# Kernel optimization log

Hardware: AMD Instinct MI355X
Metric: run time of the kernel (lower is better)

The kernel has to match this reference:

```python
import jax, jax.numpy as jnp
import numpy as np

S = 7  # output_size


def _bin_indices(lo, hi, dim):
    """PyTorch AdaptiveMaxPool windows for each of S bins over [lo, hi] (inclusive).
    Returns gather indices [R,S,K] and validity mask [R,S,K].
    start_i = floor(i*L/S), end_i = ceil((i+1)*L/S), L = hi-lo+1."""
    L = hi - lo + 1  # [R]
    i = jnp.arange(S)
    start = lo[:, None] + (i * L[:, None]) // S          # [R,S]
    end = lo[:, None] + ((i + 1) * L[:, None] + S - 1) // S  # [R,S]
    K = (dim + S - 1) // S + 1  # static max window size
    k = jnp.arange(K)
    idx = start[:, :, None] + k                          # [R,S,K]
    valid = idx < end[:, :, None]
    return jnp.clip(idx, 0, dim - 1), valid


def setup_inputs() -> dict:
    key = jax.random.key(0)
    k1, k2 = jax.random.split(key)
    feature_map = jax.random.normal(k1, (1, 256, 64, 64), dtype=jnp.float32)
    # generate valid ROIs: sort coordinate pairs so x1<=x2, y1<=y2
    pairs = jax.random.randint(k2, (1, 128, 2, 2), 0, 64)  # [B,R,(x|y),2]
    pairs = jnp.sort(pairs, axis=-1)
    rois = jnp.stack(
        [pairs[..., 0, 0], pairs[..., 1, 0], pairs[..., 0, 1], pairs[..., 1, 1]],
        axis=-1,
    ).astype(jnp.int32)  # [1,128,4] = (x1,y1,x2,y2)
    return {"feature_map": feature_map, "rois": rois}


def reference(feature_map, rois):
    f = feature_map[0]  # [C,H,W]  (module only works with batch=1)
    C, H, W = f.shape
    r = rois.reshape(-1, 4).astype(jnp.int32)
    x1, y1, x2, y2 = r[:, 0], r[:, 1], r[:, 2], r[:, 3]
    neg = jnp.finfo(f.dtype).min

    # pool over dim 2 (x / f_wid axis, per original slicing feature_map[:,:,x1:x2+1,...])
    h_idx, h_val = _bin_indices(x1, x2, H)               # [R,S,Kh]
    g1 = f[:, h_idx, :]                                  # [C,R,S,Kh,W]
    rowmax = jnp.max(jnp.where(h_val[None, :, :, :, None], g1, neg), axis=3)  # [C,R,S,W]

    # pool over dim 3 (y / f_hei axis)
    w_idx, w_val = _bin_indices(y1, y2, W)               # [R,S,Kw]
    R_, Sw, Kw = w_idx.shape
    g2 = jnp.take_along_axis(rowmax, w_idx.reshape(1, R_, 1, Sw * Kw), axis=3)
    g2 = g2.reshape(C, R_, S, Sw, Kw)                    # [C,R,S,S,Kw]
    pooled = jnp.max(jnp.where(w_val[None, :, None, :, :], g2, neg), axis=4)  # [C,R,S,S]

    # pooled_rois[b, roi, c, S, S] -> flatten to [1, R, C, S*S]
    out = pooled.transpose(1, 0, 2, 3).reshape(1, R_, C, S * S)
    return out
```

## Files before the change

### kernel.cpp

```cpp
#include <hip/hip_runtime.h>
#include <cfloat>

#define NS 7
#define NC 256
#define NH 64
#define NW 64
#define NR 128

__global__ __launch_bounds__(256) void roi_pool_kernel(
    const float* __restrict__ f,
    const int* __restrict__ rois,
    float* __restrict__ out)
{
    __shared__ float colmax_lds[4][NS][NW];

    const int lane = threadIdx.x & 63;
    const int wid  = threadIdx.x >> 6;

    const int r  = blockIdx.x >> 6;
    const int cg = blockIdx.x & 63;
    const int c  = cg * 4 + wid;

    const int x1 = rois[4 * r + 0];
    const int y1 = rois[4 * r + 1];
    const int x2 = rois[4 * r + 2];
    const int y2 = rois[4 * r + 3];
    const int Lh = x2 - x1 + 1;
    const int Lw = y2 - y1 + 1;

    const float* fc = f + (size_t)c * (NH * NW);

    for (int i = 0; i < NS; ++i) {
        const int hs = x1 + (i * Lh) / NS;
        const int he = x1 + ((i + 1) * Lh + NS - 1) / NS;
        float m = -FLT_MAX;
        if (lane < Lw) {
            const float* p = fc + hs * NW + y1 + lane;
            for (int h = hs; h < he; ++h) {
                m = fmaxf(m, *p);
                p += NW;
            }
        }
        colmax_lds[wid][i][lane] = m;
    }

    __syncthreads();

    if (lane < NS * NS) {
        const int i  = lane / NS;
        const int j  = lane % NS;
        const int cs = (j * Lw) / NS;
        const int ce = ((j + 1) * Lw + NS - 1) / NS;
        float m = -FLT_MAX;
        #pragma unroll 1
        for (int k = cs; k < ce; ++k)
            m = fmaxf(m, colmax_lds[wid][i][k]);
        out[((size_t)(r * NC + c)) * (NS * NS) + lane] = m;
    }
}

extern "C" void kernel_launch(void* const* d_in, const int* in_sizes, int n_in,
                              void* d_out, int out_size, void* d_ws, size_t ws_size,
                              hipStream_t stream)
{
    const float* feature_map = (const float*)d_in[0];
    const int*   rois        = (const int*)d_in[1];
    float*       out         = (float*)d_out;

    const int grid  = NR * (NC / 4);
    const int block = 256;

    roi_pool_kernel<<<grid, block, 0, stream>>>(feature_map, rois, out);
}
```

Before: 28.01 us.

## Process four ROIs per wave for one channel with float2 row-pair loads

Work is remapped so each block handles one channel across 16 ROIs, with each wave looping over 4 ROIs. This favours cache reuse of that channel's plane. Row pooling reads full 64-wide rows as float2, with the two half-waves taking alternate rows. The halves are merged with v_permlane32_swap, and a per-wave padded LDS stripe replaces the block-wide barrier. The cost is extra loads over the full row width regardless of ROI width, serial ROI iteration inside each wave, and a gfx950-specific inline asm instruction.

Result: slower. 30.70 us (+9.6%).

```diff
diff --git a/kernel.cpp b/kernel.cpp
--- a/kernel.cpp
+++ b/kernel.cpp
@@ -6,56 +6,95 @@
 #define NH 64
 #define NW 64
 #define NR 128
+#define SPAD 66
 
-__global__ __launch_bounds__(256) void roi_pool_kernel(
+__global__ __launch_bounds__(256, 8) void roi_pool_kernel(
     const float* __restrict__ f,
     const int* __restrict__ rois,
     float* __restrict__ out)
 {
-    __shared__ float colmax_lds[4][NS][NW];
+    __shared__ float stripe_all[4][NS][SPAD];
 
-    const int lane = threadIdx.x & 63;
-    const int wid  = threadIdx.x >> 6;
+    const int tid  = threadIdx.x;
+    const int lane = tid & 63;
+    const int wid  = tid >> 6;
+    float (*stripe)[SPAD] = stripe_all[wid];
 
-    const int r  = blockIdx.x >> 6;
-    const int cg = blockIdx.x & 63;
-    const int c  = cg * 4 + wid;
+    const int c  = blockIdx.x & 255;
+    const int rg = blockIdx.x >> 8;
+    const int r0 = rg * 16 + wid * 4;
 
-    const int x1 = rois[4 * r + 0];
-    const int y1 = rois[4 * r + 1];
-    const int x2 = rois[4 * r + 2];
-    const int y2 = rois[4 * r + 3];
-    const int Lh = x2 - x1 + 1;
-    const int Lw = y2 - y1 + 1;
+    const char* fcb = (const char*)(f + (size_t)c * (NH * NW));
 
-    const float* fc = f + (size_t)c * (NH * NW);
+    const int w2    = lane & 31;
+    const int halfb = (lane >> 5) << 8;
+    const int woff  = w2 * 8;
 
-    for (int i = 0; i < NS; ++i) {
-        const int hs = x1 + (i * Lh) / NS;
-        const int he = x1 + ((i + 1) * Lh + NS - 1) / NS;
-        float m = -FLT_MAX;
-        if (lane < Lw) {
-            const float* p = fc + hs * NW + y1 + lane;
-            for (int h = hs; h < he; ++h) {
-                m = fmaxf(m, *p);
-                p += NW;
+    const int bl = lane < NS * NS ? lane : NS * NS - 1;
+    const int bi = bl / NS;
+    const int bj = bl - bi * NS;
+
+    for (int rr = 0; rr < 4; ++rr) {
+        const int r  = r0 + rr;
+        const int x1 = __builtin_amdgcn_readfirstlane(rois[4 * r + 0]);
+        const int y1 = __builtin_amdgcn_readfirstlane(rois[4 * r + 1]);
+        const int x2 = __builtin_amdgcn_readfirstlane(rois[4 * r + 2]);
+        const int y2 = __builtin_amdgcn_readfirstlane(rois[4 * r + 3]);
+        const int Lh = x2 - x1 + 1;
+        const int Lw = y2 - y1 + 1;
+
+        int hsb[NS], helimb[NS];
+        int maxrows = 0;
+        #pragma unroll
+        for (int i = 0; i < NS; ++i) {
+            int hs = x1 + (i * Lh) / NS;
+            int he = x1 + ((i + 1) * Lh + NS - 1) / NS;
+            hsb[i]    = hs << 8;
+            helimb[i] = (he - 1) << 8;
+            maxrows   = max(maxrows, he - hs);
+        }
+        const int K2 = (maxrows + 1) >> 1;
+
+        float2 acc[NS];
+        #pragma unroll
+        for (int i = 0; i < NS; ++i) acc[i] = make_float2(-FLT_MAX, -FLT_MAX);
+
+        for (int k = 0; k < K2; ++k) {
+            const int kb = k << 9;
+            #pragma unroll
+            for (int i = 0; i < NS; ++i) {
+                int rb = min(hsb[i] + kb + halfb, helimb[i]);
+                float2 v = *(const float2*)(fcb + rb + woff);
+                acc[i].x = fmaxf(acc[i].x, v.x);
+                acc[i].y = fmaxf(acc[i].y, v.y);
             }
         }
-        colmax_lds[wid][i][lane] = m;
-    }
 
-    __syncthreads();
+        #pragma unroll
+        for (int i = 0; i < NS; ++i) {
+            float ax = acc[i].x, bx = acc[i].x;
+            float ay = acc[i].y, by = acc[i].y;
+            asm("v_permlane32_swap_b32 %0, %1" : "+v"(ax), "+v"(bx));
+            asm("v_permlane32_swap_b32 %0, %1" : "+v"(ay), "+v"(by));
+            float2 mv = make_float2(fmaxf(ax, bx), fmaxf(ay, by));
+            if (lane < 32)
+                *(float2*)&stripe[i][2 * w2] = mv;
+        }
 
-    if (lane < NS * NS) {
-        const int i  = lane / NS;
-        const int j  = lane % NS;
-        const int cs = (j * Lw) / NS;
-        const int ce = ((j + 1) * Lw + NS - 1) / NS;
-        float m = -FLT_MAX;
-        #pragma unroll 1
-        for (int k = cs; k < ce; ++k)
-            m = fmaxf(m, colmax_lds[wid][i][k]);
-        out[((size_t)(r * NC + c)) * (NS * NS) + lane] = m;
+        {
+            const int Kc  = (Lw + NS - 1) / NS;
+            const int wsj = y1 + (bj * Lw) / NS;
+            const int wej = y1 + ((bj + 1) * Lw + NS - 1) / NS;
+            const int spj = wej - wsj;
+
+            float m = -FLT_MAX;
+            for (int k = 0; k <= Kc; ++k) {
+                float v = stripe[bi][wsj + k];
+                m = fmaxf(m, k < spj ? v : -FLT_MAX);
+            }
+            if (lane < NS * NS)
+                out[((size_t)r * NC + c) * (NS * NS) + lane] = m;
+        }
     }
 }
 
@@ -67,7 +106,7 @@
     const int*   rois        = (const int*)d_in[1];
     float*       out         = (float*)d_out;
 
-    const int grid  = NR * (NC / 4);
+    const int grid  = 8 * 256;
     const int block = 256;
 
     roi_pool_kernel<<<grid, block, 0, stream>>>(feature_map, rois, out);
```

## Transpose feature map to HWC and pool one bin per wave over channels

Applied to the files above, without the earlier changes.

Adds a tiled transpose kernel that rewrites the CHW feature map into an HWC workspace. The pooling kernel then gives each wave one (roi, bin, 64-channel group), with lanes mapped to channels. Each lane reads its bin window directly with coalesced loads and no LDS or barrier. In exchange it pays an extra full transpose pass and a second launch, and the output stores become strided by 49 floats per lane.

New measurement: 32.81 us. +17.1%, slower.

```diff
diff --git a/kernel.cpp b/kernel.cpp
--- a/kernel.cpp
+++ b/kernel.cpp
@@ -7,56 +7,79 @@
 #define NW 64
 #define NR 128
 
-__global__ __launch_bounds__(256) void roi_pool_kernel(
-    const float* __restrict__ f,
-    const int* __restrict__ rois,
+#define RFL(x) __builtin_amdgcn_readfirstlane(x)
+
+__global__ __launch_bounds__(256) void transpose_chw_hwc(
+    const float* __restrict__ f, float* __restrict__ ft)
+{
+    __shared__ float tile[16][65];
+    const int tid = threadIdx.x;
+    const int h   = blockIdx.x >> 4;
+    const int c0  = ((blockIdx.x >> 2) & 3) * 64;
+    const int w0  = (blockIdx.x & 3) * 16;
+
+    {
+        int c  = tid >> 2;
+        int w4 = (tid & 3) * 4;
+        float4 v = *(const float4*)(f + (size_t)(c0 + c) * (NH * NW) + h * NW + w0 + w4);
+        tile[w4 + 0][c] = v.x;
+        tile[w4 + 1][c] = v.y;
+        tile[w4 + 2][c] = v.z;
+        tile[w4 + 3][c] = v.w;
+    }
+    __syncthreads();
+    {
+        int w  = tid >> 4;
+        int c4 = (tid & 15) * 4;
+        float4 v = make_float4(tile[w][c4 + 0], tile[w][c4 + 1],
+                               tile[w][c4 + 2], tile[w][c4 + 3]);
+        *(float4*)(ft + (size_t)h * (NW * NC) + (w0 + w) * NC + c0 + c4) = v;
+    }
+}
+
+__global__ __launch_bounds__(256) void roi_pool_hwc(
+    const float* __restrict__ ft, const int* __restrict__ rois,
     float* __restrict__ out)
 {
-    __shared__ float colmax_lds[4][NS][NW];
+    const int lane = threadIdx.x & 63;
+    const int wv   = threadIdx.x >> 6;
+    const int W    = blockIdx.x * 4 + wv;
 
-    const int lane = threadIdx.x & 63;
-    const int wid  = threadIdx.x >> 6;
+    const int cg  = RFL(W & 3);
+    const int rb_ = W >> 2;
+    const int bin = RFL(rb_ % (NS * NS));
+    const int r   = RFL(rb_ / (NS * NS));
+    const int i   = bin / NS;
+    const int j   = bin - i * NS;
 
-    const int r  = blockIdx.x >> 6;
-    const int cg = blockIdx.x & 63;
-    const int c  = cg * 4 + wid;
-
-    const int x1 = rois[4 * r + 0];
-    const int y1 = rois[4 * r + 1];
-    const int x2 = rois[4 * r + 2];
-    const int y2 = rois[4 * r + 3];
+    const int4 rq = ((const int4*)rois)[r];
+    const int x1 = RFL(rq.x), y1 = RFL(rq.y), x2 = RFL(rq.z), y2 = RFL(rq.w);
     const int Lh = x2 - x1 + 1;
     const int Lw = y2 - y1 + 1;
 
-    const float* fc = f + (size_t)c * (NH * NW);
+    const int h0 = x1 + (i * Lh) / NS;
+    const int h1 = x1 + ((i + 1) * Lh + NS - 1) / NS;
+    const int w0 = y1 + (j * Lw) / NS;
+    const int w1 = y1 + ((j + 1) * Lw + NS - 1) / NS;
 
-    for (int i = 0; i < NS; ++i) {
-        const int hs = x1 + (i * Lh) / NS;
-        const int he = x1 + ((i + 1) * Lh + NS - 1) / NS;
-        float m = -FLT_MAX;
-        if (lane < Lw) {
-            const float* p = fc + hs * NW + y1 + lane;
-            for (int h = hs; h < he; ++h) {
-                m = fmaxf(m, *p);
-                p += NW;
-            }
+    const float* fcl = ft + cg * 64 + lane;
+
+    float m = -FLT_MAX;
+    for (int h = h0; h < h1; ++h) {
+        const size_t rowo = (size_t)(h * NW) * NC;
+        for (int wg = w0; wg < w1; wg += 4) {
+            int wB = min(wg + 1, w1 - 1);
+            int wC = min(wg + 2, w1 - 1);
+            int wD = min(wg + 3, w1 - 1);
+            float a = fcl[rowo + (size_t)wg * NC];
+            float b = fcl[rowo + (size_t)wB * NC];
+            float c = fcl[rowo + (size_t)wC * NC];
+            float d = fcl[rowo + (size_t)wD * NC];
+            m = fmaxf(m, fmaxf(fmaxf(a, b), fmaxf(c, d)));
         }
-        colmax_lds[wid][i][lane] = m;
     }
 
-    __syncthreads();
-
-    if (lane < NS * NS) {
-        const int i  = lane / NS;
-        const int j  = lane % NS;
-        const int cs = (j * Lw) / NS;
-        const int ce = ((j + 1) * Lw + NS - 1) / NS;
-        float m = -FLT_MAX;
-        #pragma unroll 1
-        for (int k = cs; k < ce; ++k)
-            m = fmaxf(m, colmax_lds[wid][i][k]);
-        out[((size_t)(r * NC + c)) * (NS * NS) + lane] = m;
-    }
+    out[((size_t)(r * NC + cg * 64 + lane)) * (NS * NS) + bin] = m;
 }
 
 extern "C" void kernel_launch(void* const* d_in, const int* in_sizes, int n_in,
@@ -66,9 +89,10 @@
     const float* feature_map = (const float*)d_in[0];
     const int*   rois        = (const int*)d_in[1];
     float*       out         = (float*)d_out;
+    float*       ft          = (float*)d_ws;
 
-    const int grid  = NR * (NC / 4);
-    const int block = 256;
+    transpose_chw_hwc<<<1024, 256, 0, stream>>>(feature_map, ft);
 
-    roi_pool_kernel<<<grid, block, 0, stream>>>(feature_map, rois, out);
+    const int nwaves = NR * NS * NS * 4;
+    roi_pool_hwc<<<nwaves / 4, 256, 0, stream>>>(ft, rois, out);
 }
```
